# Kernel optimization log

Hardware: AMD Instinct MI355X
Metric: run time of the kernel (lower is better)

## Reference

```python
import jax, jax.numpy as jnp
import numpy as np

U, I, J = 256, 512, 31          # nframes, n_actions, atom_max+1
E_IN, N_EMB, N_FIT = 3, 10, 32  # len(elements)+1, N_emb, N_fit
K = N_EMB // 4                  # slice size in the descriptor einsum


def setup_inputs() -> dict:
    key = jax.random.key(0)
    ks = jax.random.split(key, 12)
    s = 0.1
    return {
        "Sg": jax.random.normal(ks[0], (U, I, J, E_IN), jnp.float32),
        "R": jax.random.normal(ks[1], (U, I, J, 4), jnp.float32),
        # mlp_emb: Linear(3,10) -> ReLU -> Linear(10,10)  (weights stored [in,out])
        "W_emb1": jax.random.normal(ks[2], (E_IN, N_EMB), jnp.float32) * s,
        "b_emb1": jax.random.normal(ks[3], (N_EMB,), jnp.float32) * s,
        "W_emb2": jax.random.normal(ks[4], (N_EMB, N_EMB), jnp.float32) * s,
        "b_emb2": jax.random.normal(ks[5], (N_EMB,), jnp.float32) * s,
        # mlp_fit: Linear(20,32) -> ReLU -> Linear(32,32) -> ReLU -> Linear(32,1)
        "W_fit1": jax.random.normal(ks[6], (K * N_EMB, N_FIT), jnp.float32) * s,
        "b_fit1": jax.random.normal(ks[7], (N_FIT,), jnp.float32) * s,
        "W_fit2": jax.random.normal(ks[8], (N_FIT, N_FIT), jnp.float32) * s,
        "b_fit2": jax.random.normal(ks[9], (N_FIT,), jnp.float32) * s,
        "W_fit3": jax.random.normal(ks[10], (N_FIT, 1), jnp.float32) * s,
        "b_fit3": jax.random.normal(ks[11], (1,), jnp.float32) * s,
    }


def reference(Sg, R, W_emb1, b_emb1, W_emb2, b_emb2,
              W_fit1, b_fit1, W_fit2, b_fit2, W_fit3, b_fit3):
    # Embedding MLP on per-neighbor species/weight vectors: [u,i,j,3] -> [u,i,j,10]
    h = jnp.maximum(Sg @ W_emb1 + b_emb1, 0.0)
    Gmat = h @ W_emb2 + b_emb2
    # Descriptor: einsum('uijk,uijl,uiml,uimn->uikn') decomposed to avoid
    # materializing the full 4-way product; sums over both neighbor dims.
    T1 = jnp.einsum('uijk,uijl->uikl', Gmat[..., :K], R)   # [u,i,2,4]
    T2 = jnp.einsum('uiml,uimn->uiln', R, Gmat)            # [u,i,4,10]
    Dmat = jnp.einsum('uikl,uiln->uikn', T1, T2)           # [u,i,2,10]
    D = Dmat.reshape(U * I, K * N_EMB)
    # Fit MLP -> scalar Q per (frame, action)
    f = jnp.maximum(D @ W_fit1 + b_fit1, 0.0)
    f = jnp.maximum(f @ W_fit2 + b_fit2, 0.0)
    Q = f @ W_fit3 + b_fit3
    return Q.reshape(U, I, 1)
```

## Files before the change

### kernel.cpp

```cpp
#include <hip/hip_runtime.h>

constexpr int J_ = 31;
constexpr int UI = 131072;
constexpr size_t D_BYTES = (size_t)UI * 20 * 4;

constexpr int PPB   = 16;
constexpr int NBLK1 = UI / PPB;

__device__ __forceinline__ float qsum(float x) {
    int a = __builtin_amdgcn_update_dpp(0, __float_as_int(x), 0xB1, 0xF, 0xF, true);
    x += __int_as_float(a);
    int b = __builtin_amdgcn_update_dpp(0, __float_as_int(x), 0x4E, 0xF, 0xF, true);
    x += __int_as_float(b);
    return x;
}

__global__ __launch_bounds__(64) void dqn_phase1(
    const float* __restrict__ Sg, const float* __restrict__ R,
    const float* __restrict__ W1, const float* __restrict__ b1,
    const float* __restrict__ W2, const float* __restrict__ b2,
    float* __restrict__ Dws)
{
    const int tid  = threadIdx.x;
    const int lp   = tid >> 2;
    const int g    = tid & 3;
    const int pair = blockIdx.x * PPB + lp;

    float w10[10], w11[10], w12[10], c1w[10];
    #pragma unroll
    for (int p = 0; p < 10; ++p) {
        w10[p] = W1[p]; w11[p] = W1[10 + p]; w12[p] = W1[20 + p]; c1w[p] = b1[p];
    }

    const float* sgp = Sg + (size_t)pair * 93 + 3 * g;
    float sA[8][3];
    #pragma unroll
    for (int b = 0; b < 8; ++b) {
        int idx = 12 * b;
        if (b == 7 && g == 3) idx = 90 - 3 * g + 12 * 0;
        const float* sp = (b == 7 && g == 3) ? (Sg + (size_t)pair * 93 + 90) : (sgp + idx);
        sA[b][0] = sp[0]; sA[b][1] = sp[1]; sA[b][2] = sp[2];
    }

    const float4* rv = reinterpret_cast<const float4*>(R + (size_t)pair * 124);
    float4 r0 = rv[g];      float4 r1 = rv[4 + g];
    float4 r2 = rv[8 + g];  float4 r3 = rv[12 + g];
    float4 r4 = rv[16 + g]; float4 r5 = rv[20 + g];
    float4 r6 = rv[24 + g];
    int jt = 28 + g;
    float4 r7 = rv[jt < J_ ? jt : (J_ - 1)];

    asm volatile("s_waitcnt vmcnt(0)" ::: "memory");
    __builtin_amdgcn_sched_barrier(0);

    float M0[10], M1[10], M2[10], M3[10];
    float4 Rs = {0.f, 0.f, 0.f, 0.f};
    #pragma unroll
    for (int p = 0; p < 10; ++p) { M0[p]=0.f; M1[p]=0.f; M2[p]=0.f; M3[p]=0.f; }

    auto PROC = [&](float s0, float s1, float s2, const float4& r4v) {
        #pragma unroll
        for (int p = 0; p < 10; ++p) {
            float t = c1w[p] + s0 * w10[p] + s1 * w11[p] + s2 * w12[p];
            t = t > 0.f ? t : 0.f;
            M0[p] += r4v.x * t;
            M1[p] += r4v.y * t;
            M2[p] += r4v.z * t;
            M3[p] += r4v.w * t;
        }
        Rs.x += r4v.x; Rs.y += r4v.y; Rs.z += r4v.z; Rs.w += r4v.w;
    };

    PROC(sA[0][0], sA[0][1], sA[0][2], r0);
    PROC(sA[1][0], sA[1][1], sA[1][2], r1);
    PROC(sA[2][0], sA[2][1], sA[2][2], r2);
    PROC(sA[3][0], sA[3][1], sA[3][2], r3);
    PROC(sA[4][0], sA[4][1], sA[4][2], r4);
    PROC(sA[5][0], sA[5][1], sA[5][2], r5);
    PROC(sA[6][0], sA[6][1], sA[6][2], r6);
    {
        float m = (g < 3) ? 1.f : 0.f;
        float4 rm = {r7.x * m, r7.y * m, r7.z * m, r7.w * m};
        PROC(sA[7][0], sA[7][1], sA[7][2], rm);
    }

    #pragma unroll
    for (int p = 0; p < 10; ++p) {
        M0[p] = qsum(M0[p]); M1[p] = qsum(M1[p]);
        M2[p] = qsum(M2[p]); M3[p] = qsum(M3[p]);
    }
    Rs.x = qsum(Rs.x); Rs.y = qsum(Rs.y); Rs.z = qsum(Rs.z); Rs.w = qsum(Rs.w);

    float Mg[10];
    #pragma unroll
    for (int p = 0; p < 10; ++p)
        Mg[p] = (g == 0) ? M0[p] : (g == 1) ? M1[p] : (g == 2) ? M2[p] : M3[p];
    float Rsg = (g == 0) ? Rs.x : (g == 1) ? Rs.y : (g == 2) ? Rs.z : Rs.w;

    float T2g[10];
    #pragma unroll
    for (int n = 0; n < 10; ++n) T2g[n] = Rsg * b2[n];
    #pragma unroll
    for (int p = 0; p < 10; ++p) {
        float m = Mg[p];
        #pragma unroll
        for (int n = 0; n < 10; ++n) T2g[n] += m * W2[p * 10 + n];
    }

    float D[20];
    #pragma unroll
    for (int k = 0; k < 2; ++k)
        #pragma unroll
        for (int n = 0; n < 10; ++n) D[k * 10 + n] = T2g[k] * T2g[n];
    #pragma unroll
    for (int t = 0; t < 20; ++t) D[t] = qsum(D[t]);

    float s0 = (g == 0) ? D[0] : (g == 1) ? D[5]  : (g == 2) ? D[10] : D[15];
    float s1 = (g == 0) ? D[1] : (g == 1) ? D[6]  : (g == 2) ? D[11] : D[16];
    float s2 = (g == 0) ? D[2] : (g == 1) ? D[7]  : (g == 2) ? D[12] : D[17];
    float s3 = (g == 0) ? D[3] : (g == 1) ? D[8]  : (g == 2) ? D[13] : D[18];
    float s4 = (g == 0) ? D[4] : (g == 1) ? D[9]  : (g == 2) ? D[14] : D[19];
    float* dw = Dws + (size_t)(g * 5) * UI + pair;
    dw[0 * UI] = s0; dw[1 * UI] = s1; dw[2 * UI] = s2;
    dw[3 * UI] = s3; dw[4 * UI] = s4;
}

__global__ __launch_bounds__(256) void dqn_phase2(
    const float* __restrict__ Dws,
    const float* __restrict__ Wf1, const float* __restrict__ bf1,
    const float* __restrict__ Wf2, const float* __restrict__ bf2,
    const float* __restrict__ Wf3, const float* __restrict__ bf3,
    float* __restrict__ out)
{
    __shared__ float4 wlds4[448];
    const int tid = threadIdx.x;

    {
        if (tid < 160) wlds4[tid] = reinterpret_cast<const float4*>(Wf1)[tid];
        wlds4[160 + tid] = reinterpret_cast<const float4*>(Wf2)[tid];
        if (tid < 8)       wlds4[416 + tid]        = reinterpret_cast<const float4*>(bf1)[tid];
        else if (tid < 16) wlds4[424 + (tid - 8)]  = reinterpret_cast<const float4*>(bf2)[tid - 8];
        else if (tid < 24) wlds4[432 + (tid - 16)] = reinterpret_cast<const float4*>(Wf3)[tid - 16];
        else if (tid == 24) { reinterpret_cast<float*>(wlds4)[1760] = bf3[0]; }
    }
    __syncthreads();

    const int gt   = blockIdx.x * 256 + tid;
    const int pair = gt >> 2;
    const int g    = gt & 3;

    float D[20];
    #pragma unroll
    for (int t = 0; t < 20; ++t) D[t] = Dws[(size_t)t * UI + pair];

    const float* wl = reinterpret_cast<const float*>(wlds4);

    float F[8];
    {
        const float4* b4 = reinterpret_cast<const float4*>(wl + 1664 + g * 8);
        float4 x = b4[0], y = b4[1];
        F[0]=x.x; F[1]=x.y; F[2]=x.z; F[3]=x.w; F[4]=y.x; F[5]=y.y; F[6]=y.z; F[7]=y.w;
    }
    #pragma unroll
    for (int kk = 0; kk < 20; ++kk) {
        float d = D[kk];
        const float4* w4 = reinterpret_cast<const float4*>(wl + kk * 32 + g * 8);
        float4 wa = w4[0], wb = w4[1];
        F[0] += d * wa.x; F[1] += d * wa.y; F[2] += d * wa.z; F[3] += d * wa.w;
        F[4] += d * wb.x; F[5] += d * wb.y; F[6] += d * wb.z; F[7] += d * wb.w;
    }
    #pragma unroll
    for (int i = 0; i < 8; ++i) F[i] = F[i] > 0.f ? F[i] : 0.f;

    float P[8];
    #pragma unroll
    for (int i = 0; i < 8; ++i) P[i] = __shfl_xor(F[i], 1);
    const bool odd = (g & 1);
    float lo[16];
    #pragma unroll
    for (int i = 0; i < 8; ++i) {
        lo[i]     = odd ? P[i] : F[i];
        lo[8 + i] = odd ? F[i] : P[i];
    }
    float hi[16];
    #pragma unroll
    for (int i = 0; i < 16; ++i) hi[i] = __shfl_xor(lo[i], 2);
    const bool up = (g & 2);
    float f1a[32];
    #pragma unroll
    for (int i = 0; i < 16; ++i) {
        f1a[i]      = up ? hi[i] : lo[i];
        f1a[16 + i] = up ? lo[i] : hi[i];
    }

    float G[8];
    {
        const float4* b4 = reinterpret_cast<const float4*>(wl + 1696 + g * 8);
        float4 x = b4[0], y = b4[1];
        G[0]=x.x; G[1]=x.y; G[2]=x.z; G[3]=x.w; G[4]=y.x; G[5]=y.y; G[6]=y.z; G[7]=y.w;
    }
    #pragma unroll
    for (int kk = 0; kk < 32; ++kk) {
        float d = f1a[kk];
        const float4* w4 = reinterpret_cast<const float4*>(wl + 640 + kk * 32 + g * 8);
        float4 wa = w4[0], wb = w4[1];
        G[0] += d * wa.x; G[1] += d * wa.y; G[2] += d * wa.z; G[3] += d * wa.w;
        G[4] += d * wb.x; G[5] += d * wb.y; G[6] += d * wb.z; G[7] += d * wb.w;
    }
    #pragma unroll
    for (int i = 0; i < 8; ++i) G[i] = G[i] > 0.f ? G[i] : 0.f;

    float qp;
    {
        const float4* w4 = reinterpret_cast<const float4*>(wl + 1728 + g * 8);
        float4 wa = w4[0], wb = w4[1];
        qp = G[0]*wa.x + G[1]*wa.y + G[2]*wa.z + G[3]*wa.w
           + G[4]*wb.x + G[5]*wb.y + G[6]*wb.z + G[7]*wb.w;
    }
    qp += __shfl_xor(qp, 1);
    qp += __shfl_xor(qp, 2);
    float q = qp + wl[1760];

    if (g == 0) out[pair] = q;
}

struct Nb1 { float s0, s1, s2; float4 r; };
__device__ __forceinline__ Nb1 load_nb1(const float* __restrict__ sg,
                                        const float* __restrict__ rr, int j) {
    Nb1 d;
    d.s0 = sg[j * 3 + 0]; d.s1 = sg[j * 3 + 1]; d.s2 = sg[j * 3 + 2];
    d.r = *reinterpret_cast<const float4*>(rr + j * 4);
    return d;
}
__global__ __launch_bounds__(256, 2) void dqn_fused_fb(
    const float* __restrict__ Sg,  const float* __restrict__ R,
    const float* __restrict__ W1,  const float* __restrict__ b1,
    const float* __restrict__ W2,  const float* __restrict__ b2,
    const float* __restrict__ Wf1, const float* __restrict__ bf1,
    const float* __restrict__ Wf2, const float* __restrict__ bf2,
    const float* __restrict__ Wf3, const float* __restrict__ bf3,
    float* __restrict__ out)
{
    const int pair = blockIdx.x * 256 + threadIdx.x;
    const float* sg = Sg + (size_t)pair * (J_ * 3);
    const float* rr = R  + (size_t)pair * (J_ * 4);
    float w1[3][10], c1[10];
    #pragma unroll
    for (int k = 0; k < 3; ++k)
        #pragma unroll
        for (int p = 0; p < 10; ++p) w1[k][p] = W1[k * 10 + p];
    #pragma unroll
    for (int p = 0; p < 10; ++p) c1[p] = b1[p];
    float M[4][10]; float Rs[4] = {0.f,0.f,0.f,0.f};
    #pragma unroll
    for (int l = 0; l < 4; ++l)
        #pragma unroll
        for (int p = 0; p < 10; ++p) M[l][p] = 0.f;
    #pragma unroll 1
    for (int j = 0; j < J_; ++j) {
        Nb1 nb = load_nb1(sg, rr, j);
        float h[10];
        #pragma unroll
        for (int p = 0; p < 10; ++p) {
            float t = c1[p] + nb.s0*w1[0][p] + nb.s1*w1[1][p] + nb.s2*w1[2][p];
            h[p] = t > 0.f ? t : 0.f;
        }
        Rs[0]+=nb.r.x; Rs[1]+=nb.r.y; Rs[2]+=nb.r.z; Rs[3]+=nb.r.w;
        #pragma unroll
        for (int p = 0; p < 10; ++p) {
            M[0][p]+=nb.r.x*h[p]; M[1][p]+=nb.r.y*h[p];
            M[2][p]+=nb.r.z*h[p]; M[3][p]+=nb.r.w*h[p];
        }
    }
    float T2[4][10];
    #pragma unroll
    for (int l = 0; l < 4; ++l)
        #pragma unroll
        for (int n = 0; n < 10; ++n) T2[l][n] = Rs[l] * b2[n];
    #pragma unroll
    for (int p = 0; p < 10; ++p) {
        #pragma unroll
        for (int l = 0; l < 4; ++l) {
            float m = M[l][p];
            #pragma unroll
            for (int n = 0; n < 10; ++n) T2[l][n] += m * W2[p * 10 + n];
        }
    }
    float D[20];
    #pragma unroll
    for (int k = 0; k < 2; ++k)
        #pragma unroll
        for (int n = 0; n < 10; ++n)
            D[k*10+n] = T2[0][k]*T2[0][n] + T2[1][k]*T2[1][n]
                      + T2[2][k]*T2[2][n] + T2[3][k]*T2[3][n];
    float f1[32];
    #pragma unroll
    for (int o = 0; o < 32; ++o) f1[o] = bf1[o];
    #pragma unroll
    for (int kk = 0; kk < 20; ++kk) {
        const float4* wrow = reinterpret_cast<const float4*>(Wf1 + kk * 32);
        float d = D[kk];
        #pragma unroll
        for (int v = 0; v < 8; ++v) {
            float4 w = wrow[v];
            f1[4*v+0]+=d*w.x; f1[4*v+1]+=d*w.y; f1[4*v+2]+=d*w.z; f1[4*v+3]+=d*w.w;
        }
    }
    #pragma unroll
    for (int o = 0; o < 32; ++o) f1[o] = f1[o] > 0.f ? f1[o] : 0.f;
    float f2[32];
    #pragma unroll
    for (int o = 0; o < 32; ++o) f2[o] = bf2[o];
    #pragma unroll
    for (int kk = 0; kk < 32; ++kk) {
        const float4* wrow = reinterpret_cast<const float4*>(Wf2 + kk * 32);
        float d = f1[kk];
        #pragma unroll
        for (int v = 0; v < 8; ++v) {
            float4 w = wrow[v];
            f2[4*v+0]+=d*w.x; f2[4*v+1]+=d*w.y; f2[4*v+2]+=d*w.z; f2[4*v+3]+=d*w.w;
        }
    }
    #pragma unroll
    for (int o = 0; o < 32; ++o) f2[o] = f2[o] > 0.f ? f2[o] : 0.f;
    float q = bf3[0];
    #pragma unroll
    for (int o = 0; o < 32; o += 4) {
        float4 w = *reinterpret_cast<const float4*>(Wf3 + o);
        q += f2[o+0]*w.x + f2[o+1]*w.y + f2[o+2]*w.z + f2[o+3]*w.w;
    }
    out[pair] = q;
}

extern "C" void kernel_launch(void* const* d_in, const int* in_sizes, int n_in,
                              void* d_out, int out_size, void* d_ws, size_t ws_size,
                              hipStream_t stream) {
    const float* Sg  = (const float*)d_in[0];
    const float* R   = (const float*)d_in[1];
    const float* W1  = (const float*)d_in[2];
    const float* b1  = (const float*)d_in[3];
    const float* W2  = (const float*)d_in[4];
    const float* b2  = (const float*)d_in[5];
    const float* Wf1 = (const float*)d_in[6];
    const float* bf1 = (const float*)d_in[7];
    const float* Wf2 = (const float*)d_in[8];
    const float* bf2 = (const float*)d_in[9];
    const float* Wf3 = (const float*)d_in[10];
    const float* bf3 = (const float*)d_in[11];
    float* out = (float*)d_out;

    if (ws_size >= D_BYTES) {
        float* Dws = (float*)d_ws;
        dqn_phase1<<<dim3(NBLK1), dim3(64), 0, stream>>>(
            Sg, R, W1, b1, W2, b2, Dws);
        dqn_phase2<<<dim3((UI * 4) / 256), dim3(256), 0, stream>>>(
            Dws, Wf1, bf1, Wf2, bf2, Wf3, bf3, out);
    } else {
        dqn_fused_fb<<<dim3(UI / 256), dim3(256), 0, stream>>>(
            Sg, R, W1, b1, W2, b2, Wf1, bf1, Wf2, bf2, Wf3, bf3, out);
    }
}
```

Measured before the change: 42.94 us.

## Process two pair tiles per block in phase1 with prefetched second tile

Each phase1 block now handles two consecutive tiles of 16 pairs instead of one, halving the grid. Loads for the second tile are issued partway through computing the first. An explicit vmcnt wait then lets the first tile's stores stay outstanding while the second tile is computed. The aim is to hide global-load latency inside a wave, at the cost of higher register pressure and possibly lower occupancy.

```diff
diff --git a/kernel.cpp b/kernel.cpp
--- a/kernel.cpp
+++ b/kernel.cpp
@@ -4,8 +4,8 @@
 constexpr int UI = 131072;
 constexpr size_t D_BYTES = (size_t)UI * 20 * 4;
 
-constexpr int PPB   = 16;
-constexpr int NBLK1 = UI / PPB;
+constexpr int PPT   = 16;
+constexpr int NBLK1 = UI / (PPT * 2);
 
 __device__ __forceinline__ float qsum(float x) {
     int a = __builtin_amdgcn_update_dpp(0, __float_as_int(x), 0xB1, 0xF, 0xF, true);
@@ -21,10 +21,13 @@
     const float* __restrict__ W2, const float* __restrict__ b2,
     float* __restrict__ Dws)
 {
-    const int tid  = threadIdx.x;
-    const int lp   = tid >> 2;
-    const int g    = tid & 3;
-    const int pair = blockIdx.x * PPB + lp;
+    const int tid = threadIdx.x;
+    const int lp  = tid >> 2;
+    const int g   = tid & 3;
+
+    const int t0    = blockIdx.x * 2;
+    const int pair0 = t0 * PPT + lp;
+    const int pair1 = pair0 + PPT;
 
     float w10[10], w11[10], w12[10], c1w[10];
     #pragma unroll
@@ -32,33 +35,34 @@
         w10[p] = W1[p]; w11[p] = W1[10 + p]; w12[p] = W1[20 + p]; c1w[p] = b1[p];
     }
 
-    const float* sgp = Sg + (size_t)pair * 93 + 3 * g;
-    float sA[8][3];
-    #pragma unroll
-    for (int b = 0; b < 8; ++b) {
-        int idx = 12 * b;
-        if (b == 7 && g == 3) idx = 90 - 3 * g + 12 * 0;
-        const float* sp = (b == 7 && g == 3) ? (Sg + (size_t)pair * 93 + 90) : (sgp + idx);
-        sA[b][0] = sp[0]; sA[b][1] = sp[1]; sA[b][2] = sp[2];
-    }
-
-    const float4* rv = reinterpret_cast<const float4*>(R + (size_t)pair * 124);
-    float4 r0 = rv[g];      float4 r1 = rv[4 + g];
-    float4 r2 = rv[8 + g];  float4 r3 = rv[12 + g];
-    float4 r4 = rv[16 + g]; float4 r5 = rv[20 + g];
-    float4 r6 = rv[24 + g];
-    int jt = 28 + g;
-    float4 r7 = rv[jt < J_ ? jt : (J_ - 1)];
-
-    asm volatile("s_waitcnt vmcnt(0)" ::: "memory");
-    __builtin_amdgcn_sched_barrier(0);
+    auto SGLOAD = [&](int pair, float (&s)[8][3]) {
+        const float* sgp = Sg + (size_t)pair * 93 + 3 * g;
+        #pragma unroll
+        for (int b = 0; b < 8; ++b) {
+            const float* sp = (b == 7 && g == 3)
+                            ? (Sg + (size_t)pair * 93 + 90) : (sgp + 12 * b);
+            s[b][0] = sp[0]; s[b][1] = sp[1]; s[b][2] = sp[2];
+        }
+    };
+    auto RLOAD = [&](int pair, float4& r0, float4& r1, float4& r2, float4& r3,
+                     float4& r4, float4& r5, float4& r6, float4& r7) {
+        const float4* rv = reinterpret_cast<const float4*>(R + (size_t)pair * 124);
+        r0 = rv[g];      r1 = rv[4 + g];  r2 = rv[8 + g];  r3 = rv[12 + g];
+        r4 = rv[16 + g]; r5 = rv[20 + g]; r6 = rv[24 + g];
+        int jt = 28 + g;
+        r7 = rv[jt < J_ ? jt : (J_ - 1)];
+    };
 
     float M0[10], M1[10], M2[10], M3[10];
-    float4 Rs = {0.f, 0.f, 0.f, 0.f};
-    #pragma unroll
-    for (int p = 0; p < 10; ++p) { M0[p]=0.f; M1[p]=0.f; M2[p]=0.f; M3[p]=0.f; }
-
-    auto PROC = [&](float s0, float s1, float s2, const float4& r4v) {
+    float4 Rs;
+
+    auto INIT = [&]() {
+        Rs = make_float4(0.f, 0.f, 0.f, 0.f);
+        #pragma unroll
+        for (int p = 0; p < 10; ++p) { M0[p]=0.f; M1[p]=0.f; M2[p]=0.f; M3[p]=0.f; }
+    };
+    auto PROC = [&](const float (&s)[3], const float4& r4v) {
+        float s0 = s[0], s1 = s[1], s2 = s[2];
         #pragma unroll
         for (int p = 0; p < 10; ++p) {
             float t = c1w[p] + s0 * w10[p] + s1 * w11[p] + s2 * w12[p];
@@ -70,59 +74,81 @@
         }
         Rs.x += r4v.x; Rs.y += r4v.y; Rs.z += r4v.z; Rs.w += r4v.w;
     };
-
-    PROC(sA[0][0], sA[0][1], sA[0][2], r0);
-    PROC(sA[1][0], sA[1][1], sA[1][2], r1);
-    PROC(sA[2][0], sA[2][1], sA[2][2], r2);
-    PROC(sA[3][0], sA[3][1], sA[3][2], r3);
-    PROC(sA[4][0], sA[4][1], sA[4][2], r4);
-    PROC(sA[5][0], sA[5][1], sA[5][2], r5);
-    PROC(sA[6][0], sA[6][1], sA[6][2], r6);
-    {
+    auto TAIL = [&](const float (&s)[3], const float4& r7) {
         float m = (g < 3) ? 1.f : 0.f;
         float4 rm = {r7.x * m, r7.y * m, r7.z * m, r7.w * m};
-        PROC(sA[7][0], sA[7][1], sA[7][2], rm);
-    }
-
-    #pragma unroll
-    for (int p = 0; p < 10; ++p) {
-        M0[p] = qsum(M0[p]); M1[p] = qsum(M1[p]);
-        M2[p] = qsum(M2[p]); M3[p] = qsum(M3[p]);
-    }
-    Rs.x = qsum(Rs.x); Rs.y = qsum(Rs.y); Rs.z = qsum(Rs.z); Rs.w = qsum(Rs.w);
-
-    float Mg[10];
-    #pragma unroll
-    for (int p = 0; p < 10; ++p)
-        Mg[p] = (g == 0) ? M0[p] : (g == 1) ? M1[p] : (g == 2) ? M2[p] : M3[p];
-    float Rsg = (g == 0) ? Rs.x : (g == 1) ? Rs.y : (g == 2) ? Rs.z : Rs.w;
-
-    float T2g[10];
-    #pragma unroll
-    for (int n = 0; n < 10; ++n) T2g[n] = Rsg * b2[n];
-    #pragma unroll
-    for (int p = 0; p < 10; ++p) {
-        float m = Mg[p];
-        #pragma unroll
-        for (int n = 0; n < 10; ++n) T2g[n] += m * W2[p * 10 + n];
-    }
-
-    float D[20];
-    #pragma unroll
-    for (int k = 0; k < 2; ++k)
-        #pragma unroll
-        for (int n = 0; n < 10; ++n) D[k * 10 + n] = T2g[k] * T2g[n];
-    #pragma unroll
-    for (int t = 0; t < 20; ++t) D[t] = qsum(D[t]);
-
-    float s0 = (g == 0) ? D[0] : (g == 1) ? D[5]  : (g == 2) ? D[10] : D[15];
-    float s1 = (g == 0) ? D[1] : (g == 1) ? D[6]  : (g == 2) ? D[11] : D[16];
-    float s2 = (g == 0) ? D[2] : (g == 1) ? D[7]  : (g == 2) ? D[12] : D[17];
-    float s3 = (g == 0) ? D[3] : (g == 1) ? D[8]  : (g == 2) ? D[13] : D[18];
-    float s4 = (g == 0) ? D[4] : (g == 1) ? D[9]  : (g == 2) ? D[14] : D[19];
-    float* dw = Dws + (size_t)(g * 5) * UI + pair;
-    dw[0 * UI] = s0; dw[1 * UI] = s1; dw[2 * UI] = s2;
-    dw[3 * UI] = s3; dw[4 * UI] = s4;
+        PROC(s, rm);
+    };
+    auto FINISH = [&](int pair) {
+        #pragma unroll
+        for (int p = 0; p < 10; ++p) {
+            M0[p] = qsum(M0[p]); M1[p] = qsum(M1[p]);
+            M2[p] = qsum(M2[p]); M3[p] = qsum(M3[p]);
+        }
+        Rs.x = qsum(Rs.x); Rs.y = qsum(Rs.y); Rs.z = qsum(Rs.z); Rs.w = qsum(Rs.w);
+
+        float Mg[10];
+        #pragma unroll
+        for (int p = 0; p < 10; ++p)
+            Mg[p] = (g == 0) ? M0[p] : (g == 1) ? M1[p] : (g == 2) ? M2[p] : M3[p];
+        float Rsg = (g == 0) ? Rs.x : (g == 1) ? Rs.y : (g == 2) ? Rs.z : Rs.w;
+
+        float T2g[10];
+        #pragma unroll
+        for (int n = 0; n < 10; ++n) T2g[n] = Rsg * b2[n];
+        #pragma unroll
+        for (int p = 0; p < 10; ++p) {
+            float m = Mg[p];
+            #pragma unroll
+            for (int n = 0; n < 10; ++n) T2g[n] += m * W2[p * 10 + n];
+        }
+
+        float D[20];
+        #pragma unroll
+        for (int k = 0; k < 2; ++k)
+            #pragma unroll
+            for (int n = 0; n < 10; ++n) D[k * 10 + n] = T2g[k] * T2g[n];
+        #pragma unroll
+        for (int t = 0; t < 20; ++t) D[t] = qsum(D[t]);
+
+        float s0 = (g == 0) ? D[0] : (g == 1) ? D[5]  : (g == 2) ? D[10] : D[15];
+        float s1 = (g == 0) ? D[1] : (g == 1) ? D[6]  : (g == 2) ? D[11] : D[16];
+        float s2 = (g == 0) ? D[2] : (g == 1) ? D[7]  : (g == 2) ? D[12] : D[17];
+        float s3 = (g == 0) ? D[3] : (g == 1) ? D[8]  : (g == 2) ? D[13] : D[18];
+        float s4 = (g == 0) ? D[4] : (g == 1) ? D[9]  : (g == 2) ? D[14] : D[19];
+        float* dw = Dws + (size_t)(g * 5) * UI + pair;
+        dw[0 * UI] = s0; dw[1 * UI] = s1; dw[2 * UI] = s2;
+        dw[3 * UI] = s3; dw[4 * UI] = s4;
+    };
+
+    float sA[8][3];
+    float4 a0,a1,a2,a3,a4,a5,a6,a7;
+    SGLOAD(pair0, sA);
+    RLOAD(pair0, a0,a1,a2,a3,a4,a5,a6,a7);
+    asm volatile("s_waitcnt vmcnt(0)" ::: "memory");
+    __builtin_amdgcn_sched_barrier(0);
+
+    INIT();
+    PROC(sA[0], a0); PROC(sA[1], a1); PROC(sA[2], a2); PROC(sA[3], a3);
+
+    float sB[8][3];
+    float4 q0,q1,q2,q3,q4,q5,q6,q7;
+    SGLOAD(pair1, sB);
+    RLOAD(pair1, q0,q1,q2,q3,q4,q5,q6,q7);
+    __builtin_amdgcn_sched_barrier(0);
+
+    PROC(sA[4], a4); PROC(sA[5], a5); PROC(sA[6], a6);
+    TAIL(sA[7], a7);
+    FINISH(pair0);
+
+    asm volatile("s_waitcnt vmcnt(5)" ::: "memory");
+    __builtin_amdgcn_sched_barrier(0);
+
+    INIT();
+    PROC(sB[0], q0); PROC(sB[1], q1); PROC(sB[2], q2); PROC(sB[3], q3);
+    PROC(sB[4], q4); PROC(sB[5], q5); PROC(sB[6], q6);
+    TAIL(sB[7], q7);
+    FINISH(pair1);
 }
 
 __global__ __launch_bounds__(256) void dqn_phase2(
```

New measurement: 43.62 us. About the same (+1.6%).
